# Optimization experiments

Measured on AMD Instinct MI355X. Metric: run time of the kernel, lower is better.

## Reference

```python
import jax, jax.numpy as jnp
import numpy as np

D, H, DK, DF = 512, 8, 64, 2048  # dim, heads, head_dim, forward_dim
EPS = 1e-5


def _layernorm(x, g, b):
    mu = jnp.mean(x, axis=-1, keepdims=True)
    var = jnp.mean(jnp.square(x - mu), axis=-1, keepdims=True)
    return (x - mu) * jax.lax.rsqrt(var + EPS) * g + b


def setup_inputs() -> dict:
    key = jax.random.key(0)
    ks = jax.random.split(key, 16)
    B, S = 2, 2048
    s_in = 1.0 / np.sqrt(D)
    s_ff = 1.0 / np.sqrt(DF)
    s_cat = 1.0 / np.sqrt(H * DK)
    return {
        "x": jax.random.normal(ks[0], (B, S, D), jnp.float32),
        # per-head Q/K/V projections stacked over heads: [H, D, DK]
        "Wq": jax.random.uniform(ks[1], (H, D, DK), jnp.float32, -s_in, s_in),
        "bq": jax.random.uniform(ks[2], (H, DK), jnp.float32, -s_in, s_in),
        "Wk": jax.random.uniform(ks[3], (H, D, DK), jnp.float32, -s_in, s_in),
        "bk": jax.random.uniform(ks[4], (H, DK), jnp.float32, -s_in, s_in),
        "Wv": jax.random.uniform(ks[5], (H, D, DK), jnp.float32, -s_in, s_in),
        "bv": jax.random.uniform(ks[6], (H, DK), jnp.float32, -s_in, s_in),
        "Wo": jax.random.uniform(ks[7], (H * DK, D), jnp.float32, -s_cat, s_cat),
        "bo": jax.random.uniform(ks[8], (D,), jnp.float32, -s_cat, s_cat),
        "ln1_g": jnp.ones((D,), jnp.float32),
        "ln1_b": jnp.zeros((D,), jnp.float32),
        "W1": jax.random.uniform(ks[9], (D, DF), jnp.float32, -s_in, s_in),
        "b1": jax.random.uniform(ks[10], (DF,), jnp.float32, -s_in, s_in),
        "W2": jax.random.uniform(ks[11], (DF, D), jnp.float32, -s_ff, s_ff),
        "b2": jax.random.uniform(ks[12], (D,), jnp.float32, -s_ff, s_ff),
        "ln2_g": jnp.ones((D,), jnp.float32),
        "ln2_b": jnp.zeros((D,), jnp.float32),
    }


def reference(x, Wq, bq, Wk, bk, Wv, bv, Wo, bo, ln1_g, ln1_b, W1, b1, W2, b2, ln2_g, ln2_b):
    # Per-head projections, batched over heads: [B,H,S,DK]
    q = jnp.einsum('bsd,hdk->bhsk', x, Wq) + bq[None, :, None, :]
    k = jnp.einsum('bsd,hdk->bhsk', x, Wk) + bk[None, :, None, :]
    v = jnp.einsum('bsd,hdk->bhsk', x, Wv) + bv[None, :, None, :]
    scale = 1.0 / np.sqrt(DK)
    scores = jnp.einsum('bhsk,bhtk->bhst', q, k) * scale  # [B,H,S,S]
    attn = jax.nn.softmax(scores, axis=-1)
    o = jnp.einsum('bhst,bhtk->bhsk', attn, v)  # [B,H,S,DK]
    # concat heads (head order matches torch cat over ModuleList)
    B, _, S, _ = o.shape
    o = o.transpose(0, 2, 1, 3).reshape(B, S, H * DK)
    attn_out = o @ Wo + bo
    # Residual 1 (dropout = identity in eval): LN(x + sublayer(x))
    h = _layernorm(x + attn_out, ln1_g, ln1_b)
    # FeedForward + Residual 2
    ff = jax.nn.relu(h @ W1 + b1) @ W2 + b2
    return _layernorm(h + ff, ln2_g, ln2_b)
```

## Files before the change

### kernel.cpp

```cpp
#include <hip/hip_runtime.h>


#define Dm   512
#define Hh   8
#define DKk  64
#define DFf  2048
#define Bb   2
#define Ss   2048
#define Nn   4096

typedef __attribute__((ext_vector_type(8))) short short8;
typedef __attribute__((ext_vector_type(4))) float f32x4;
typedef __attribute__((ext_vector_type(2))) float f32x2;
typedef __attribute__((ext_vector_type(4))) short short4v;
typedef __attribute__((ext_vector_type(2))) int   int2v;

__device__ inline float bf2f(short s) {
    unsigned u = ((unsigned)(unsigned short)s) << 16;
    float f; __builtin_memcpy(&f, &u, 4); return f;
}
__device__ inline void bf2x2(unsigned v, float& a, float& b) {
    unsigned ua = v << 16, ub = v & 0xffff0000u;
    __builtin_memcpy(&a, &ua, 4); __builtin_memcpy(&b, &ub, 4);
}
__device__ inline short f2bf(float f) {
    unsigned u; __builtin_memcpy(&u, &f, 4);
    u = (u + 0x7fff + ((u >> 16) & 1)) >> 16;
    return (short)u;
}
__device__ inline short cvt_elem(const void* p, long i, int f32flag) {
    if (f32flag) return f2bf(((const float*)p)[i]);
    return ((const short*)p)[i];
}
__device__ inline int detect_f32(const void* x) {
    const float* xf = (const float*)x;
    int ok = 0;
#pragma unroll
    for (int i = 0; i < 16; ++i) {
        float a = fabsf(xf[i]);
        ok += (a > 1e-8f && a < 1e4f) ? 1 : 0;
    }
    return ok >= 8;
}
__device__ inline void gload_lds16(const short* g, short* l) {
    __builtin_amdgcn_global_load_lds(
        (const __attribute__((address_space(1))) unsigned int*)g,
        (__attribute__((address_space(3))) unsigned int*)l, 16, 0, 0);
}

__global__ __launch_bounds__(256) void prep_kernel(
    const void* __restrict__ x, short* __restrict__ xb,
    const void* bq, const void* bk, const void* bv, const void* bo,
    const void* b1, const void* b2, const void* g1, const void* be1,
    const void* g2, const void* be2, short* __restrict__ smalls,
    const void* Wq, const void* Wk, const void* Wv,
    const void* Wo, const void* W1, const void* W2,
    short* __restrict__ WqkvT,
    short* __restrict__ WoT, short* __restrict__ W1T, short* __restrict__ W2T)
{
    const int f = detect_f32(x);
    int blk = blockIdx.x;
    if (blk < 512) {
        long base = (long)blk * 4096;
        if (f) {
            const float* xf = (const float*)x;
#pragma unroll
            for (int j = 0; j < 4; ++j) {
                int off = threadIdx.x * 4 + j * 1024;
                f32x4 v = *(const f32x4*)(xf + base + off);
                short4v s4;
#pragma unroll
                for (int i2 = 0; i2 < 4; ++i2) s4[i2] = f2bf(v[i2]);
                *(short4v*)(xb + base + off) = s4;
            }
        } else {
            const short* xs = (const short*)x;
#pragma unroll
            for (int j = 0; j < 2; ++j) {
                int off = threadIdx.x * 8 + j * 2048;
                *(short8*)(xb + base + off) = *(const short8*)(xs + base + off);
            }
        }
        return;
    }
    if (blk == 512) {
        const void* srcs[10] = {bq, bk, bv, bo, b1, b2, g1, be1, g2, be2};
        const int   sz[10]   = {512, 512, 512, 512, 2048, 512, 512, 512, 512, 512};
        int off = 0;
        for (int j = 0; j < 10; ++j) {
            for (int i = threadIdx.x; i < sz[j]; i += 256)
                smalls[off + i] = cvt_elem(srcs[j], i, f);
            off += sz[j];
        }
        return;
    }
    __shared__ short tile[64][65];
    blk -= 513;
    const void* src; short* dst; long srcoff = 0; long dstoff = 0; int R, C, tr, tc;
    if (blk < 192) {
        int m = blk >> 6; int r = blk & 63; int h = r >> 3; int t = r & 7;
        src = (m == 0) ? Wq : (m == 1) ? Wk : Wv;
        dst = WqkvT + (long)m * 512 * 512;
        srcoff = (long)h * 512 * 64; dstoff = (long)h * 64 * 512;
        R = 512; C = 64; tr = t; tc = 0;
    } else if (blk < 256) {
        int r = blk - 192; src = Wo; dst = WoT; R = 512; C = 512; tr = r >> 3; tc = r & 7;
    } else if (blk < 512) {
        int r = blk - 256; src = W1; dst = W1T; R = 512; C = 2048; tr = r >> 5; tc = r & 31;
    } else {
        int r = blk - 512; src = W2; dst = W2T; R = 2048; C = 512; tr = r >> 3; tc = r & 7;
    }
    int r0 = tr * 64, c0 = tc * 64;
    for (int i = threadIdx.x; i < 4096; i += 256) {
        int rr = i >> 6, cc = i & 63;
        tile[rr][cc] = cvt_elem(src, srcoff + (long)(r0 + rr) * C + c0 + cc, f);
    }
    __syncthreads();
    for (int i = threadIdx.x; i < 4096; i += 256) {
        int cc = i >> 6, rr = i & 63;
        dst[dstoff + (long)(c0 + cc) * R + r0 + rr] = tile[rr][cc];
    }
}

#define MODE_PART_BF16 1
#define MODE_RELU_BF16 2
#define MODE_QKV       4

#define QSCALE 0.18033688011112042f

__global__ __launch_bounds__(256) void gemm_kernel(
    const short* __restrict__ A, const short* __restrict__ Bt,
    const short* __restrict__ bias, void* __restrict__ outp,
    void* __restrict__ out2, void* __restrict__ out3,
    int K, int Ncols, int mode, int Ktile)
{
    __shared__ short As[2][128 * 64];
    __shared__ short Bs[2][128 * 64];
    const int t    = threadIdx.x;
    const int lane = t & 63;
    const int wave = t >> 6;
    const int quad = lane >> 4;
    const int l15  = lane & 15;
    const int wm = wave >> 1, wn = wave & 1;
    const int row0 = blockIdx.x * 128;
    const int col0 = blockIdx.y * 128;
    const int kbase = blockIdx.z * Ktile;

    const int ri = lane >> 3;
    const int ct = (lane & 7) ^ ri;

    f32x4 acc[4][4];
#pragma unroll
    for (int i = 0; i < 4; ++i)
#pragma unroll
        for (int j = 0; j < 4; ++j) acc[i][j] = (f32x4){0.f, 0.f, 0.f, 0.f};

    auto stage = [&](int buf, int k0) {
#pragma unroll
        for (int p = 0; p < 4; ++p) {
            int r = wave * 32 + p * 8;
            gload_lds16(A + (long)(row0 + r + ri) * K + kbase + k0 + ct * 8,
                        &As[buf][r * 64 + lane * 8]);
        }
#pragma unroll
        for (int p = 0; p < 4; ++p) {
            int r = wave * 32 + p * 8;
            gload_lds16(Bt + (long)(col0 + r + ri) * K + kbase + k0 + ct * 8,
                        &Bs[buf][r * 64 + lane * 8]);
        }
    };

    stage(0, 0);
    int cur = 0;
    const int niter = Ktile >> 6;
    for (int it = 0; it < niter; ++it) {
        asm volatile("s_waitcnt vmcnt(0)" ::: "memory");
        __syncthreads();
        if (it + 1 < niter) stage(cur ^ 1, (it + 1) * 64);
#pragma unroll
        for (int kk = 0; kk < 2; ++kk) {
            short8 af[4], bfr[4];
#pragma unroll
            for (int mt = 0; mt < 4; ++mt) {
                int rowa = wm * 64 + mt * 16 + l15;
                af[mt] = *(const short8*)&As[cur][rowa * 64
                              + (((kk * 4 + quad) ^ (rowa & 7)) * 8)];
            }
#pragma unroll
            for (int nt = 0; nt < 4; ++nt) {
                int rowb = wn * 64 + nt * 16 + l15;
                bfr[nt] = *(const short8*)&Bs[cur][rowb * 64
                              + (((kk * 4 + quad) ^ (rowb & 7)) * 8)];
            }
#pragma unroll
            for (int mt = 0; mt < 4; ++mt)
#pragma unroll
                for (int nt = 0; nt < 4; ++nt)
                    acc[mt][nt] = __builtin_amdgcn_mfma_f32_16x16x32_bf16(
                        af[mt], bfr[nt], acc[mt][nt], 0, 0, 0);
        }
        cur ^= 1;
    }

    const int wrow0 = row0 + wm * 64;
    const int wcol0 = col0 + wn * 64;
    if (mode == MODE_QKV) {
        int m = wcol0 >> 9;
        if (m < 2) {
            short* out = (short*)(m == 0 ? outp : out2);
            float sc = (m == 0) ? QSCALE : 1.0f;
#pragma unroll
            for (int nt = 0; nt < 4; ++nt) {
                int col = wcol0 + nt * 16 + l15;
                float bb = bf2f(bias[col]);
                int cl = col & 511;
#pragma unroll
                for (int mt = 0; mt < 4; ++mt)
#pragma unroll
                    for (int r = 0; r < 4; ++r) {
                        int row = wrow0 + mt * 16 + quad * 4 + r;
                        out[(long)row * 512 + cl] = f2bf((acc[mt][nt][r] + bb) * sc);
                    }
            }
        } else {
            short* out = (short*)out3;
#pragma unroll
            for (int nt = 0; nt < 4; ++nt) {
                int col = wcol0 + nt * 16 + l15;
                float bb = bf2f(bias[col]);
                int cl = col - 1024;
                int h = cl >> 6, kk = cl & 63;
#pragma unroll
                for (int mt = 0; mt < 4; ++mt) {
                    int row = wrow0 + mt * 16 + quad * 4;
                    int b = row >> 11, s = row & 2047;
                    short4v v4;
#pragma unroll
                    for (int r = 0; r < 4; ++r) v4[r] = f2bf(acc[mt][nt][r] + bb);
                    *(short4v*)&out[((long)(b * Hh + h) * DKk + kk) * Ss + s] = v4;
                }
            }
        }
    } else if (mode == MODE_PART_BF16) {
        short* out = (short*)outp + (long)blockIdx.z * Nn * Ncols;
        int zb = (blockIdx.z == 0);
#pragma unroll
        for (int nt = 0; nt < 4; ++nt) {
            int col = wcol0 + nt * 16 + l15;
            float bb = zb ? bf2f(bias[col]) : 0.f;
#pragma unroll
            for (int mt = 0; mt < 4; ++mt)
#pragma unroll
                for (int r = 0; r < 4; ++r) {
                    int row = wrow0 + mt * 16 + quad * 4 + r;
                    out[(long)row * Ncols + col] = f2bf(acc[mt][nt][r] + bb);
                }
        }
    } else {
        short* out = (short*)outp;
#pragma unroll
        for (int nt = 0; nt < 4; ++nt) {
            int col = wcol0 + nt * 16 + l15;
            float bb = bf2f(bias[col]);
#pragma unroll
            for (int mt = 0; mt < 4; ++mt)
#pragma unroll
                for (int r = 0; r < 4; ++r) {
                    int row = wrow0 + mt * 16 + quad * 4 + r;
                    out[(long)row * Ncols + col] = f2bf(fmaxf(acc[mt][nt][r] + bb, 0.f));
                }
        }
    }
}

__global__ __launch_bounds__(256) void wo_gemm_kernel(
    const short* __restrict__ po, const float* __restrict__ ls,
    const short* __restrict__ Bt, const short* __restrict__ bias,
    short* __restrict__ outp)
{
    __shared__ short As[2][128 * 64];
    __shared__ short Bs[2][128 * 64];
    const int t    = threadIdx.x;
    const int lane = t & 63;
    const int wave = t >> 6;
    const int quad = lane >> 4;
    const int l15  = lane & 15;
    const int wm = wave >> 1, wn = wave & 1;
    const int row0 = blockIdx.x * 128;
    const int col0 = blockIdx.y * 128;
    const int z    = blockIdx.z;
    const int b    = row0 >> 11;
    const int qtl  = (row0 >> 7) & 15;

    const int ri = lane >> 3;
    const int ct = (lane & 7) ^ ri;

    f32x4 acc[4][4];
#pragma unroll
    for (int i = 0; i < 4; ++i)
#pragma unroll
        for (int j = 0; j < 4; ++j) acc[i][j] = (f32x4){0.f, 0.f, 0.f, 0.f};

    auto stageB = [&](int buf, int k0) {
#pragma unroll
        for (int p = 0; p < 4; ++p) {
            int r = wave * 32 + p * 8;
            gload_lds16(Bt + (long)(col0 + r + ri) * Dm + z * 256 + k0 + ct * 8,
                        &Bs[buf][r * 64 + lane * 8]);
        }
    };

    short8 pv[4][4];
    float  Lv[4];
    auto loadA = [&](int it) {
        int h = z * 4 + it;
        long tb = ((long)((b * Hh + h) * 16 + qtl)) * 4;
        const short* pob = po + tb * 128 * 64;
        const float* lsb = ls + tb * 128;
#pragma unroll
        for (int p = 0; p < 4; ++p) {
            int q = wave * 32 + p * 8 + ri;
            float L = 0.f;
#pragma unroll
            for (int ks = 0; ks < 4; ++ks) {
                pv[p][ks] = *(const short8*)(pob + ((long)ks * 128 + q) * 64 + ct * 8);
                L += lsb[ks * 128 + q];
            }
            Lv[p] = L;
        }
    };
    auto finishA = [&](int buf) {
#pragma unroll
        for (int p = 0; p < 4; ++p) {
            int r = wave * 32 + p * 8;
            float inv = 1.f / Lv[p];
            short8 a8;
#pragma unroll
            for (int e = 0; e < 8; ++e) {
                float s = bf2f(pv[p][0][e]) + bf2f(pv[p][1][e])
                        + bf2f(pv[p][2][e]) + bf2f(pv[p][3][e]);
                a8[e] = f2bf(s * inv);
            }
            *(short8*)&As[buf][r * 64 + lane * 8] = a8;
        }
    };

    loadA(0);
    stageB(0, 0);
    finishA(0);
    int cur = 0;
    for (int it = 0; it < 4; ++it) {
        asm volatile("s_waitcnt vmcnt(0)" ::: "memory");
        __syncthreads();
        if (it < 3) {
            loadA(it + 1);
            stageB(cur ^ 1, (it + 1) * 64);
        }
#pragma unroll
        for (int kk = 0; kk < 2; ++kk) {
            short8 af[4], bfr[4];
#pragma unroll
            for (int mt = 0; mt < 4; ++mt) {
                int rowa = wm * 64 + mt * 16 + l15;
                af[mt] = *(const short8*)&As[cur][rowa * 64
                              + (((kk * 4 + quad) ^ (rowa & 7)) * 8)];
            }
#pragma unroll
            for (int nt = 0; nt < 4; ++nt) {
                int rowb = wn * 64 + nt * 16 + l15;
                bfr[nt] = *(const short8*)&Bs[cur][rowb * 64
                              + (((kk * 4 + quad) ^ (rowb & 7)) * 8)];
            }
#pragma unroll
            for (int mt = 0; mt < 4; ++mt)
#pragma unroll
                for (int nt = 0; nt < 4; ++nt)
                    acc[mt][nt] = __builtin_amdgcn_mfma_f32_16x16x32_bf16(
                        af[mt], bfr[nt], acc[mt][nt], 0, 0, 0);
        }
        if (it < 3) finishA(cur ^ 1);
        cur ^= 1;
    }

    const int wrow0 = row0 + wm * 64;
    const int wcol0 = col0 + wn * 64;
    short* out = outp + (long)z * Nn * Dm;
    int zb = (z == 0);
#pragma unroll
    for (int nt = 0; nt < 4; ++nt) {
        int col = wcol0 + nt * 16 + l15;
        float bb = zb ? bf2f(bias[col]) : 0.f;
#pragma unroll
        for (int mt = 0; mt < 4; ++mt)
#pragma unroll
            for (int r = 0; r < 4; ++r) {
                int row = wrow0 + mt * 16 + quad * 4 + r;
                out[(long)row * Dm + col] = f2bf(acc[mt][nt][r] + bb);
            }
    }
}

__global__ __launch_bounds__(256) void attn_kernel(
    const short* __restrict__ Q, const short* __restrict__ Kt,
    const short* __restrict__ Vt, short* __restrict__ po, float* __restrict__ ls)
{
    __shared__ __align__(16) short Ks[64 * 64];
    __shared__ __align__(16) short Vs[64 * 64];
    __shared__ __align__(16) short pbuf[4][32 * 72];
    const int lane = threadIdx.x & 63;
    const int wave = threadIdx.x >> 6;
    const int quad = lane >> 4;
    const int l15  = lane & 15;
    const int qt = blockIdx.x, bh = blockIdx.y, ks = blockIdx.z;
    const int b = bh >> 3, h = bh & 7;
    const int qrow = b * Ss + qt * 128 + wave * 32;

    short8 bq[2][2];
#pragma unroll
    for (int qh = 0; qh < 2; ++qh)
#pragma unroll
        for (int kk = 0; kk < 2; ++kk)
            bq[qh][kk] = *(const short8*)(Q + (long)(qrow + qh * 16 + l15) * Dm
                                          + h * DKk + kk * 32 + quad * 8);

    short8 ones;
#pragma unroll
    for (int i = 0; i < 8; ++i) ones[i] = (short)0x3F80;

    f32x4 o[2][4];
    f32x4 olsum[2];
#pragma unroll
    for (int qh = 0; qh < 2; ++qh) {
        olsum[qh] = (f32x4){0.f, 0.f, 0.f, 0.f};
#pragma unroll
        for (int nt = 0; nt < 4; ++nt) o[qh][nt] = (f32x4){0.f, 0.f, 0.f, 0.f};
    }

    const short* Kg = Kt + (long)b * Ss * Dm + h * DKk;
    const short* Vg = Vt + (long)bh * DKk * Ss;
    short* pbw = pbuf[wave];
    const int t00 = ks * 512;

    const int ri = lane >> 3;
    const int ct = (lane & 7) ^ ri;
    const int ldsrow0 = wave * 16;

    for (int it = 0; it < 8; ++it) {
        const int t0 = t00 + it * 64;
#pragma unroll
        for (int p = 0; p < 2; ++p) {
            int r = ldsrow0 + p * 8 + ri;
            gload_lds16(Kg + (long)(t0 + r) * Dm + ct * 8,
                        &Ks[(ldsrow0 + p * 8) * 64] + lane * 8);
        }
#pragma unroll
        for (int p = 0; p < 2; ++p) {
            int r = ldsrow0 + p * 8 + ri;
            gload_lds16(Vg + (long)r * Ss + t0 + ct * 8,
                        &Vs[(ldsrow0 + p * 8) * 64] + lane * 8);
        }
        asm volatile("s_waitcnt vmcnt(0)" ::: "memory");
        __syncthreads();

#pragma unroll
        for (int j = 0; j < 4; ++j) {
            short8 kf0 = *(const short8*)&Ks[(j * 16 + l15) * 64
                                             + ((quad ^ (l15 & 7)) * 8)];
            short8 kf1 = *(const short8*)&Ks[(j * 16 + l15) * 64
                                             + (((4 + quad) ^ (l15 & 7)) * 8)];
#pragma unroll
            for (int qh = 0; qh < 2; ++qh) {
                f32x4 sj = (f32x4){0.f, 0.f, 0.f, 0.f};
                sj = __builtin_amdgcn_mfma_f32_16x16x32_bf16(kf0, bq[qh][0], sj, 0, 0, 0);
                sj = __builtin_amdgcn_mfma_f32_16x16x32_bf16(kf1, bq[qh][1], sj, 0, 0, 0);
                int2v pk;
#pragma unroll
                for (int r2 = 0; r2 < 2; ++r2) {
                    float pa = __builtin_amdgcn_exp2f(sj[r2 * 2 + 0]);
                    float pc = __builtin_amdgcn_exp2f(sj[r2 * 2 + 1]);
                    unsigned ua, uc;
                    __builtin_memcpy(&ua, &pa, 4);
                    __builtin_memcpy(&uc, &pc, 4);
                    pk[r2] = __builtin_amdgcn_perm(uc, ua, 0x07060302);
                }
                *(int2v*)&pbw[(qh * 16 + l15) * 72 + j * 16 + quad * 4] = pk;
            }
        }
        asm volatile("s_waitcnt lgkmcnt(0)" ::: "memory");
#pragma unroll
        for (int c = 0; c < 2; ++c) {
            short8 ap[2];
#pragma unroll
            for (int qh = 0; qh < 2; ++qh) {
                ap[qh] = *(const short8*)&pbw[(qh * 16 + l15) * 72 + c * 32 + quad * 8];
                olsum[qh] = __builtin_amdgcn_mfma_f32_16x16x32_bf16(
                    ap[qh], ones, olsum[qh], 0, 0, 0);
            }
#pragma unroll
            for (int nt = 0; nt < 4; ++nt) {
                short8 vf = *(const short8*)&Vs[(nt * 16 + l15) * 64
                                                + (((c * 4 + quad) ^ (l15 & 7)) * 8)];
#pragma unroll
                for (int qh = 0; qh < 2; ++qh)
                    o[qh][nt] = __builtin_amdgcn_mfma_f32_16x16x32_bf16(
                        ap[qh], vf, o[qh][nt], 0, 0, 0);
            }
        }
        asm volatile("" ::: "memory");
        __syncthreads();
    }

    short* pob = po + ((((long)bh * 16 + qt) * 4 + ks) * 128) * 64;
#pragma unroll
    for (int qh = 0; qh < 2; ++qh)
#pragma unroll
        for (int nt = 0; nt < 4; ++nt)
#pragma unroll
            for (int r = 0; r < 4; ++r)
                pob[(wave * 32 + qh * 16 + quad * 4 + r) * 64 + nt * 16 + l15] =
                    f2bf(o[qh][nt][r]);
    if (l15 == 0) {
        long lbase = (((long)bh * 16 + qt) * 4 + ks) * 128 + wave * 32;
#pragma unroll
        for (int qh = 0; qh < 2; ++qh)
            *(f32x4*)&ls[lbase + qh * 16 + quad * 4] = olsum[qh];
    }
}

__global__ __launch_bounds__(256) void ln_kernel(
    const short* __restrict__ v0, const short* __restrict__ v1,
    const short* __restrict__ v2, const short* __restrict__ v3,
    const short* res,
    const short* __restrict__ g, const short* __restrict__ bt,
    void* out, const void* __restrict__ xdet)
{
    const int row = blockIdx.x, tid = threadIdx.x;
    const long base = (long)row * Dm;
    const int e0 = tid * 2;
    float x0, x1;
    { unsigned v = *(const unsigned*)(res + base + e0); bf2x2(v, x0, x1); }
    { unsigned v = *(const unsigned*)(v0 + base + e0);
      float a, c; bf2x2(v, a, c); x0 += a; x1 += c; }
    if (v1) { unsigned v = *(const unsigned*)(v1 + base + e0);
              float a, c; bf2x2(v, a, c); x0 += a; x1 += c; }
    if (v2) { unsigned v = *(const unsigned*)(v2 + base + e0);
              float a, c; bf2x2(v, a, c); x0 += a; x1 += c; }
    if (v3) { unsigned v = *(const unsigned*)(v3 + base + e0);
              float a, c; bf2x2(v, a, c); x0 += a; x1 += c; }

    __shared__ float red[8];
    const int wv = tid >> 6, ln = tid & 63;
    float s = x0 + x1;
#pragma unroll
    for (int mk = 1; mk < 64; mk <<= 1) s += __shfl_xor(s, mk);
    if (!ln) red[wv] = s;
    __syncthreads();
    float mean = (red[0] + red[1] + red[2] + red[3]) * (1.f / 512.f);
    float d0 = x0 - mean, d1 = x1 - mean;
    float q = d0 * d0 + d1 * d1;
#pragma unroll
    for (int mk = 1; mk < 64; mk <<= 1) q += __shfl_xor(q, mk);
    if (!ln) red[4 + wv] = q;
    __syncthreads();
    float rs = rsqrtf((red[4] + red[5] + red[6] + red[7]) * (1.f / 512.f) + 1e-5f);
    float ga, gb, ba, bb;
    { unsigned v = *(const unsigned*)(g + e0);  bf2x2(v, ga, gb); }
    { unsigned v = *(const unsigned*)(bt + e0); bf2x2(v, ba, bb); }
    float y0 = d0 * rs * ga + ba;
    float y1 = d1 * rs * gb + bb;
    int f32out = xdet ? detect_f32(xdet) : 0;
    if (f32out) {
        *(f32x2*)((float*)out + base + e0) = (f32x2){y0, y1};
    } else {
        short* o = (short*)out;
        unsigned pk = (unsigned)(unsigned short)f2bf(y0)
                    | ((unsigned)(unsigned short)f2bf(y1) << 16);
        *(unsigned*)(o + base + e0) = pk;
    }
}

extern "C" void kernel_launch(void* const* d_in, const int* in_sizes, int n_in,
                              void* d_out, int out_size, void* d_ws, size_t ws_size,
                              hipStream_t stream)
{
    (void)in_sizes; (void)n_in; (void)out_size; (void)ws_size;
    const void* x   = d_in[0];
    const void* Wq  = d_in[1];  const void* bq  = d_in[2];
    const void* Wk  = d_in[3];  const void* bk  = d_in[4];
    const void* Wv  = d_in[5];  const void* bv  = d_in[6];
    const void* Wo  = d_in[7];  const void* bo  = d_in[8];
    const void* g1  = d_in[9];  const void* be1 = d_in[10];
    const void* W1  = d_in[11]; const void* b1  = d_in[12];
    const void* W2  = d_in[13]; const void* b2  = d_in[14];
    const void* g2  = d_in[15]; const void* be2 = d_in[16];

    char* ws = (char*)d_ws;
    size_t off = 0;
    auto alloc = [&](size_t bytes) -> void* {
        void* p = ws + off; off += (bytes + 255) & ~(size_t)255; return p;
    };
    short* WqkvT = (short*)alloc((size_t)3 * Dm * Dm * 2);
    short* WoT   = (short*)alloc((size_t)Dm * Dm * 2);
    short* W1T   = (short*)alloc((size_t)DFf * Dm * 2);
    short* W2T   = (short*)alloc((size_t)Dm * DFf * 2);
    short* xb    = (short*)alloc((size_t)Nn * Dm * 2);
    short* sm    = (short*)alloc((size_t)6656 * 2);
    char*  regA  = (char*)alloc((size_t)Nn * DFf * 2);
    short* Qb    = (short*)(regA);
    short* Kb    = (short*)(regA + (size_t)Nn * Dm * 2);
    short* Vt    = (short*)(regA + (size_t)Nn * Dm * 4);
    short* u     = (short*)(regA);
    char*  regC  = (char*)alloc((size_t)4 * Nn * Dm * 2 * 2);
    short* po    = (short*)regC;
    short* f2p   = (short*)regC;
    short* wo_p  = (short*)alloc((size_t)2 * Nn * Dm * 2);
    float* lsb   = (float*)alloc((size_t)16 * 16 * 4 * 128 * 4);
    short* h_bf  = xb;

    prep_kernel<<<1281, 256, 0, stream>>>(x, xb, bq, bk, bv, bo, b1, b2,
                                          g1, be1, g2, be2, sm,
                                          Wq, Wk, Wv, Wo, W1, W2,
                                          WqkvT, WoT, W1T, W2T);
    gemm_kernel<<<dim3(Nn / 128, 1536 / 128, 1), 256, 0, stream>>>(
        xb, WqkvT, sm + 0, Qb, Kb, Vt, Dm, 1536, MODE_QKV, Dm);
    attn_kernel<<<dim3(Ss / 128, Bb * Hh, 4), 256, 0, stream>>>(Qb, Kb, Vt, po, lsb);
    wo_gemm_kernel<<<dim3(Nn / 128, Dm / 128, 2), 256, 0, stream>>>(
        po, lsb, WoT, sm + 1536, wo_p);
    ln_kernel<<<Nn, 256, 0, stream>>>(wo_p, wo_p + (long)Nn * Dm, nullptr, nullptr,
                                      xb, sm + 4608, sm + 5120, h_bf, nullptr);
    gemm_kernel<<<dim3(Nn / 128, DFf / 128, 1), 256, 0, stream>>>(
        h_bf, W1T, sm + 2048, u, nullptr, nullptr, Dm, DFf, MODE_RELU_BF16, Dm);
    gemm_kernel<<<dim3(Nn / 128, Dm / 128, 4), 256, 0, stream>>>(
        u, W2T, sm + 4096, f2p, nullptr, nullptr, DFf, Dm, MODE_PART_BF16, DFf / 4);
    ln_kernel<<<Nn, 256, 0, stream>>>(f2p, f2p + (long)Nn * Dm, f2p + (long)2 * Nn * Dm,
                                      f2p + (long)3 * Nn * Dm,
                                      h_bf, sm + 5632, sm + 6144, d_out, x);
}
```

Before: 199.4 us.

## Split Wo GEMM over four head groups and vectorize weight transpose

The Wo projection GEMM is split into four K-partitions of two heads each instead of two partitions of four heads. This doubles the grid and halves the serial loop per block, and the following LayerNorm kernel now sums four partial outputs. The partial buffer is aliased onto the unused regA region instead of getting its own workspace allocation. Separately, the prep transpose now loads with f32x4/short8 vectors and stores short4 vectors instead of scalar elements. The cost is extra partial-sum traffic into the LN kernel.

```diff
diff --git a/kernel.cpp b/kernel.cpp
--- a/kernel.cpp
+++ b/kernel.cpp
@@ -111,14 +111,36 @@
         int r = blk - 512; src = W2; dst = W2T; R = 2048; C = 512; tr = r >> 3; tc = r & 7;
     }
     int r0 = tr * 64, c0 = tc * 64;
-    for (int i = threadIdx.x; i < 4096; i += 256) {
-        int rr = i >> 6, cc = i & 63;
-        tile[rr][cc] = cvt_elem(src, srcoff + (long)(r0 + rr) * C + c0 + cc, f);
+    if (f) {
+        const float* sf = (const float*)src;
+#pragma unroll
+        for (int j = 0; j < 4; ++j) {
+            int i = threadIdx.x * 4 + j * 1024;
+            int rr = i >> 6, cc = i & 63;
+            f32x4 v = *(const f32x4*)(sf + srcoff + (long)(r0 + rr) * C + c0 + cc);
+#pragma unroll
+            for (int e = 0; e < 4; ++e) tile[rr][cc + e] = f2bf(v[e]);
+        }
+    } else {
+        const short* sp = (const short*)src;
+#pragma unroll
+        for (int j = 0; j < 2; ++j) {
+            int i = threadIdx.x * 8 + j * 2048;
+            int rr = i >> 6, cc = i & 63;
+            short8 v = *(const short8*)(sp + srcoff + (long)(r0 + rr) * C + c0 + cc);
+#pragma unroll
+            for (int e = 0; e < 8; ++e) tile[rr][cc + e] = v[e];
+        }
     }
     __syncthreads();
-    for (int i = threadIdx.x; i < 4096; i += 256) {
-        int cc = i >> 6, rr = i & 63;
-        dst[dstoff + (long)(c0 + cc) * R + r0 + rr] = tile[rr][cc];
+#pragma unroll
+    for (int j = 0; j < 4; ++j) {
+        int cc = (threadIdx.x >> 4) + 16 * j;
+        int rr0 = (threadIdx.x & 15) * 4;
+        short4v s4;
+#pragma unroll
+        for (int e = 0; e < 4; ++e) s4[e] = tile[rr0 + e][cc];
+        *(short4v*)(dst + dstoff + (long)(c0 + cc) * R + r0 + rr0) = s4;
     }
 }
 
@@ -305,7 +327,7 @@
 #pragma unroll
         for (int p = 0; p < 4; ++p) {
             int r = wave * 32 + p * 8;
-            gload_lds16(Bt + (long)(col0 + r + ri) * Dm + z * 256 + k0 + ct * 8,
+            gload_lds16(Bt + (long)(col0 + r + ri) * Dm + z * 128 + k0 + ct * 8,
                         &Bs[buf][r * 64 + lane * 8]);
         }
     };
@@ -313,7 +335,7 @@
     short8 pv[4][4];
     float  Lv[4];
     auto loadA = [&](int it) {
-        int h = z * 4 + it;
+        int h = z * 2 + it;
         long tb = ((long)((b * Hh + h) * 16 + qtl)) * 4;
         const short* pob = po + tb * 128 * 64;
         const float* lsb = ls + tb * 128;
@@ -349,10 +371,10 @@
     stageB(0, 0);
     finishA(0);
     int cur = 0;
-    for (int it = 0; it < 4; ++it) {
+    for (int it = 0; it < 2; ++it) {
         asm volatile("s_waitcnt vmcnt(0)" ::: "memory");
         __syncthreads();
-        if (it < 3) {
+        if (it < 1) {
             loadA(it + 1);
             stageB(cur ^ 1, (it + 1) * 64);
         }
@@ -378,7 +400,7 @@
                     acc[mt][nt] = __builtin_amdgcn_mfma_f32_16x16x32_bf16(
                         af[mt], bfr[nt], acc[mt][nt], 0, 0, 0);
         }
-        if (it < 3) finishA(cur ^ 1);
+        if (it < 1) finishA(cur ^ 1);
         cur ^= 1;
     }
 
@@ -610,10 +632,10 @@
     short* Kb    = (short*)(regA + (size_t)Nn * Dm * 2);
     short* Vt    = (short*)(regA + (size_t)Nn * Dm * 4);
     short* u     = (short*)(regA);
+    short* wo_p  = (short*)(regA);
     char*  regC  = (char*)alloc((size_t)4 * Nn * Dm * 2 * 2);
     short* po    = (short*)regC;
     short* f2p   = (short*)regC;
-    short* wo_p  = (short*)alloc((size_t)2 * Nn * Dm * 2);
     float* lsb   = (float*)alloc((size_t)16 * 16 * 4 * 128 * 4);
     short* h_bf  = xb;
 
@@ -624,9 +646,11 @@
     gemm_kernel<<<dim3(Nn / 128, 1536 / 128, 1), 256, 0, stream>>>(
         xb, WqkvT, sm + 0, Qb, Kb, Vt, Dm, 1536, MODE_QKV, Dm);
     attn_kernel<<<dim3(Ss / 128, Bb * Hh, 4), 256, 0, stream>>>(Qb, Kb, Vt, po, lsb);
-    wo_gemm_kernel<<<dim3(Nn / 128, Dm / 128, 2), 256, 0, stream>>>(
+    wo_gemm_kernel<<<dim3(Nn / 128, Dm / 128, 4), 256, 0, stream>>>(
         po, lsb, WoT, sm + 1536, wo_p);
-    ln_kernel<<<Nn, 256, 0, stream>>>(wo_p, wo_p + (long)Nn * Dm, nullptr, nullptr,
+    ln_kernel<<<Nn, 256, 0, stream>>>(wo_p, wo_p + (long)Nn * Dm,
+                                      wo_p + (long)2 * Nn * Dm,
+                                      wo_p + (long)3 * Nn * Dm,
                                       xb, sm + 4608, sm + 5120, h_bf, nullptr);
     gemm_kernel<<<dim3(Nn / 128, DFf / 128, 1), 256, 0, stream>>>(
         h_bf, W1T, sm + 2048, u, nullptr, nullptr, Dm, DFf, MODE_RELU_BF16, Dm);
```

New measurement: 205.5 us. 1.03x slower.
